# Kernel optimization log

Hardware: AMD Instinct MI355X
Metric: run time of the kernel (lower is better)

## Reference

```python
import jax, jax.numpy as jnp
import numpy as np

NNZ = 819200
VOCAB = 1000000
EMBED = 64
BATCH = 4096


def setup_inputs() -> dict:
    key = jax.random.key(0)
    k1, k2, k3, k4 = jax.random.split(key, 4)
    feature_embedding = jax.random.normal(k1, (VOCAB, EMBED), dtype=jnp.float32) * 0.05
    feature_vals = jax.random.uniform(k2, (NNZ,), dtype=jnp.float32)
    batch_ids = jnp.sort(jax.random.randint(k3, (NNZ,), 0, BATCH, dtype=jnp.int32))
    feat_ids = jax.random.randint(k4, (NNZ,), 0, VOCAB, dtype=jnp.int32)
    return {
        "feature_embedding": feature_embedding,
        "feature_vals": feature_vals,
        "batch_ids": batch_ids,
        "feat_ids": feat_ids,
        "batch_size": BATCH,
    }


def reference(feature_embedding, feature_vals, batch_ids, feat_ids, batch_size):
    # Gather embedding rows for each nonzero (sparse_dense_matmul == gather + segment_sum)
    emb = feature_embedding[feat_ids]                      # [nnz, D]
    v = feature_vals[:, None]                              # [nnz, 1]
    # sum over features per batch row of v * e, then square
    s = jax.ops.segment_sum(v * emb, batch_ids, num_segments=batch_size)       # [B, D]
    sum_square = s * s
    # sum over features per batch row of v^2 * e^2
    square_sum = jax.ops.segment_sum((v * v) * (emb * emb), batch_ids,
                                     num_segments=batch_size)                   # [B, D]
    return 0.5 * (sum_square - square_sum)
```

## Files before the change

kernel.cpp:

```cpp
#include <hip/hip_runtime.h>

#define EMBED 64
#define BATCH 4096

__global__ __launch_bounds__(256) void fm_kernel(
    const float* __restrict__ emb,
    const float* __restrict__ vals,
    const int*   __restrict__ bids,
    const int*   __restrict__ fids,
    float*       __restrict__ out,
    int nnz)
{
    const int wave_in_block = threadIdx.x >> 6;
    const int lane          = threadIdx.x & 63;
    const int row           = blockIdx.x * 4 + wave_in_block;
    if (row >= BATCH) return;

    int lo = 0, hi = nnz;
    while (lo < hi) {
        int mid = (lo + hi) >> 1;
        if (bids[mid] < row) lo = mid + 1; else hi = mid;
    }
    const int start = lo;
    hi = nnz;
    while (lo < hi) {
        int mid = (lo + hi) >> 1;
        if (bids[mid] < row + 1) lo = mid + 1; else hi = mid;
    }
    const int end = lo;

    float s = 0.f, sq = 0.f;
    int i = start;
    for (; i + 4 <= end; i += 4) {
        float v0 = vals[i + 0], v1 = vals[i + 1], v2 = vals[i + 2], v3 = vals[i + 3];
        int   f0 = fids[i + 0], f1 = fids[i + 1], f2 = fids[i + 2], f3 = fids[i + 3];
        float e0 = emb[(size_t)f0 * EMBED + lane];
        float e1 = emb[(size_t)f1 * EMBED + lane];
        float e2 = emb[(size_t)f2 * EMBED + lane];
        float e3 = emb[(size_t)f3 * EMBED + lane];
        float a0 = v0 * e0, a1 = v1 * e1, a2 = v2 * e2, a3 = v3 * e3;
        s  += (a0 + a1) + (a2 + a3);
        sq += (a0 * a0 + a1 * a1) + (a2 * a2 + a3 * a3);
    }
    for (; i < end; ++i) {
        float v = vals[i];
        int   f = fids[i];
        float e = emb[(size_t)f * EMBED + lane];
        float a = v * e;
        s  += a;
        sq += a * a;
    }

    out[(size_t)row * EMBED + lane] = 0.5f * (s * s - sq);
}

extern "C" void kernel_launch(void* const* d_in, const int* in_sizes, int n_in,
                              void* d_out, int out_size, void* d_ws, size_t ws_size,
                              hipStream_t stream) {
    const float* emb  = (const float*)d_in[0];
    const float* vals = (const float*)d_in[1];
    const int*   bids = (const int*)d_in[2];
    const int*   fids = (const int*)d_in[3];
    float*       out  = (float*)d_out;
    const int nnz = in_sizes[1];

    const int rows_per_block = 4;
    const int blocks = (BATCH + rows_per_block - 1) / rows_per_block;
    fm_kernel<<<dim3(blocks), dim3(256), 0, stream>>>(emb, vals, bids, fids, out, nnz);
}
```

Baseline: 369.8 us.

## Split segment-sum over fixed nnz chunks with atomic partials and finalize kernel

Replaces the one-wave-per-batch-row design, which needs a binary search and only 4096 waves, with one wave per 128-nonzero chunk. Each 16-lane group gathers float4 embedding slices for 8 nonzeros at once, accumulates sum and square-sum per run of equal batch ids, and flushes them to workspace buffers with atomicAdd. A memset and a small finalize kernel then compute 0.5*(s^2 - q). The goal is more parallelism and memory-level parallelism for the random gathers, at the cost of extra launches, atomics at chunk boundaries, and nondeterministic float summation order.

Result: slower. 384.7 us (+4.0%).

```diff
diff --git a/kernel.cpp b/kernel.cpp
--- a/kernel.cpp
+++ b/kernel.cpp
@@ -2,69 +2,116 @@
 
 #define EMBED 64
 #define BATCH 4096
+#define CHUNK 128
+#define G     8
 
-__global__ __launch_bounds__(256) void fm_kernel(
-    const float* __restrict__ emb,
-    const float* __restrict__ vals,
-    const int*   __restrict__ bids,
-    const int*   __restrict__ fids,
-    float*       __restrict__ out,
+__global__ __launch_bounds__(256) void fm_accum(
+    const float4* __restrict__ emb4,
+    const float*  __restrict__ vals,
+    const int*    __restrict__ bids,
+    const int*    __restrict__ fids,
+    float* __restrict__ s_buf,
+    float* __restrict__ q_buf,
     int nnz)
 {
-    const int wave_in_block = threadIdx.x >> 6;
-    const int lane          = threadIdx.x & 63;
-    const int row           = blockIdx.x * 4 + wave_in_block;
-    if (row >= BATCH) return;
+    const int gid  = blockIdx.x * blockDim.x + threadIdx.x;
+    const int wave = gid >> 6;
+    const int lane = threadIdx.x & 63;
+    const int grp  = lane >> 4;
+    const int sub  = lane & 15;
 
-    int lo = 0, hi = nnz;
-    while (lo < hi) {
-        int mid = (lo + hi) >> 1;
-        if (bids[mid] < row) lo = mid + 1; else hi = mid;
+    const int base = wave * CHUNK;
+    if (base >= nnz) return;
+    const int end = min(base + CHUNK, nnz);
+
+    float4 s = make_float4(0.f, 0.f, 0.f, 0.f);
+    float4 q = make_float4(0.f, 0.f, 0.f, 0.f);
+    int cur = -1;
+
+    for (int it = base; it < end; it += 4 * G) {
+        int r[G]; float v[G]; int f[G]; float4 e[G];
+
+        #pragma unroll
+        for (int g = 0; g < G; ++g) {
+            int i   = it + 4 * g + grp;
+            bool ok = (i < end);
+            int idx = ok ? i : end - 1;
+            r[g] = bids[idx];
+            f[g] = fids[idx];
+            v[g] = ok ? vals[idx] : 0.f;
+        }
+        #pragma unroll
+        for (int g = 0; g < G; ++g)
+            e[g] = emb4[(size_t)f[g] * 16 + sub];
+
+        #pragma unroll
+        for (int g = 0; g < G; ++g) {
+            if (r[g] != cur) {
+                if (cur >= 0) {
+                    float* sp = s_buf + (size_t)cur * EMBED + (sub << 2);
+                    float* qp = q_buf + (size_t)cur * EMBED + (sub << 2);
+                    atomicAdd(sp + 0, s.x); atomicAdd(sp + 1, s.y);
+                    atomicAdd(sp + 2, s.z); atomicAdd(sp + 3, s.w);
+                    atomicAdd(qp + 0, q.x); atomicAdd(qp + 1, q.y);
+                    atomicAdd(qp + 2, q.z); atomicAdd(qp + 3, q.w);
+                }
+                cur = r[g];
+                s = make_float4(0.f, 0.f, 0.f, 0.f);
+                q = make_float4(0.f, 0.f, 0.f, 0.f);
+            }
+            float ax = v[g] * e[g].x, ay = v[g] * e[g].y;
+            float az = v[g] * e[g].z, aw = v[g] * e[g].w;
+            s.x += ax;      s.y += ay;      s.z += az;      s.w += aw;
+            q.x += ax * ax; q.y += ay * ay; q.z += az * az; q.w += aw * aw;
+        }
     }
-    const int start = lo;
-    hi = nnz;
-    while (lo < hi) {
-        int mid = (lo + hi) >> 1;
-        if (bids[mid] < row + 1) lo = mid + 1; else hi = mid;
+    if (cur >= 0) {
+        float* sp = s_buf + (size_t)cur * EMBED + (sub << 2);
+        float* qp = q_buf + (size_t)cur * EMBED + (sub << 2);
+        atomicAdd(sp + 0, s.x); atomicAdd(sp + 1, s.y);
+        atomicAdd(sp + 2, s.z); atomicAdd(sp + 3, s.w);
+        atomicAdd(qp + 0, q.x); atomicAdd(qp + 1, q.y);
+        atomicAdd(qp + 2, q.z); atomicAdd(qp + 3, q.w);
     }
-    const int end = lo;
+}
 
-    float s = 0.f, sq = 0.f;
-    int i = start;
-    for (; i + 4 <= end; i += 4) {
-        float v0 = vals[i + 0], v1 = vals[i + 1], v2 = vals[i + 2], v3 = vals[i + 3];
-        int   f0 = fids[i + 0], f1 = fids[i + 1], f2 = fids[i + 2], f3 = fids[i + 3];
-        float e0 = emb[(size_t)f0 * EMBED + lane];
-        float e1 = emb[(size_t)f1 * EMBED + lane];
-        float e2 = emb[(size_t)f2 * EMBED + lane];
-        float e3 = emb[(size_t)f3 * EMBED + lane];
-        float a0 = v0 * e0, a1 = v1 * e1, a2 = v2 * e2, a3 = v3 * e3;
-        s  += (a0 + a1) + (a2 + a3);
-        sq += (a0 * a0 + a1 * a1) + (a2 * a2 + a3 * a3);
+__global__ __launch_bounds__(256) void fm_final(
+    const float4* __restrict__ sb, const float4* __restrict__ qb,
+    float4* __restrict__ out, int n4)
+{
+    int i = blockIdx.x * blockDim.x + threadIdx.x;
+    if (i < n4) {
+        float4 s = sb[i], q = qb[i], o;
+        o.x = 0.5f * (s.x * s.x - q.x);
+        o.y = 0.5f * (s.y * s.y - q.y);
+        o.z = 0.5f * (s.z * s.z - q.z);
+        o.w = 0.5f * (s.w * s.w - q.w);
+        out[i] = o;
     }
-    for (; i < end; ++i) {
-        float v = vals[i];
-        int   f = fids[i];
-        float e = emb[(size_t)f * EMBED + lane];
-        float a = v * e;
-        s  += a;
-        sq += a * a;
-    }
-
-    out[(size_t)row * EMBED + lane] = 0.5f * (s * s - sq);
 }
 
 extern "C" void kernel_launch(void* const* d_in, const int* in_sizes, int n_in,
                               void* d_out, int out_size, void* d_ws, size_t ws_size,
                               hipStream_t stream) {
-    const float* emb  = (const float*)d_in[0];
-    const float* vals = (const float*)d_in[1];
-    const int*   bids = (const int*)d_in[2];
-    const int*   fids = (const int*)d_in[3];
-    float*       out  = (float*)d_out;
+    const float4* emb4 = (const float4*)d_in[0];
+    const float*  vals = (const float*)d_in[1];
+    const int*    bids = (const int*)d_in[2];
+    const int*    fids = (const int*)d_in[3];
+    float*        out  = (float*)d_out;
     const int nnz = in_sizes[1];
 
-    const int rows_per_block = 4;
-    const int blocks = (BATCH + rows_per_block - 1) / rows_per_block;
-    fm_kernel<<<dim3(blocks), dim3(256), 0, stream>>>(emb, vals, bids, fids, out, nnz);
+    float* s_buf = (float*)d_ws;
+    float* q_buf = s_buf + (size_t)BATCH * EMBED;
+
+    hipMemsetAsync(d_ws, 0, (size_t)BATCH * EMBED * 2 * sizeof(float), stream);
+
+    const int waves   = (nnz + CHUNK - 1) / CHUNK;
+    const int threads = waves * 64;
+    const int blocks  = (threads + 255) / 256;
+    fm_accum<<<dim3(blocks), dim3(256), 0, stream>>>(emb4, vals, bids, fids,
+                                                     s_buf, q_buf, nnz);
+
+    const int n4 = BATCH * EMBED / 4;
+    fm_final<<<dim3((n4 + 255) / 256), dim3(256), 0, stream>>>(
+        (const float4*)s_buf, (const float4*)q_buf, (float4*)out, n4);
 }
```
